# Kernel tuning notes

Measured on AMD Instinct MI355X. Metric: run time of the kernel, lower is better.

Reference implementation:

```python
import jax, jax.numpy as jnp
import numpy as np

D_MODEL = 512
D_STATE = 16
EPS = 1e-8
LN_EPS = 1e-5


def setup_inputs() -> dict:
    key = jax.random.key(0)
    ks = jax.random.split(key, 9)
    B, N = 4, 2048
    x = jax.random.normal(ks[0], (B, N, D_MODEL), dtype=jnp.float32)
    A_log = jax.random.normal(ks[1], (D_STATE,), dtype=jnp.float32) * 0.1 - 1.0
    # xavier_uniform with gain=0.5 for B and C linear weights
    lim_B = 0.5 * np.sqrt(6.0 / (D_MODEL + D_STATE))
    W_B = jax.random.uniform(ks[2], (D_STATE, D_MODEL), jnp.float32, -lim_B, lim_B)
    W_C = jax.random.uniform(ks[3], (D_MODEL, D_STATE), jnp.float32, -lim_B, lim_B)
    D = jax.random.normal(ks[4], (D_MODEL,), dtype=jnp.float32) * 0.01
    lim_g = np.sqrt(1.0 / D_MODEL)  # torch Linear default init
    W_gate = jax.random.uniform(ks[5], (D_MODEL, D_MODEL), jnp.float32, -lim_g, lim_g)
    b_gate = jax.random.uniform(ks[6], (D_MODEL,), jnp.float32, -lim_g, lim_g)
    ln_gamma = jnp.ones((D_MODEL,), jnp.float32)
    ln_beta = jnp.zeros((D_MODEL,), jnp.float32)
    return {"x": x, "A_log": A_log, "W_B": W_B, "W_C": W_C, "D": D,
            "W_gate": W_gate, "b_gate": b_gate, "ln_gamma": ln_gamma, "ln_beta": ln_beta}


def reference(x, A_log, W_B, W_C, D, W_gate, b_gate, ln_gamma, ln_beta):
    Bb, N, Dm = x.shape
    A = -jnp.clip(jnp.exp(A_log), EPS, 10.0)                      # (d_state,)
    dt = 1.0 / N
    A_bar = jnp.exp(dt * A)                                       # (d_state,)
    B_bar = jnp.where(jnp.abs(A) > EPS, (A_bar - 1.0) / (A + EPS),
                      jnp.full_like(A, dt))
    Bu = jnp.einsum('bnm,sm->bns', x, W_B) * B_bar                # (B,N,d_state)
    idx = jnp.arange(N)
    diff = jnp.clip(idx[None, :] - idx[:, None], 0, None)[..., None]  # (N,N,1)
    decay = A_bar[None, None, :] ** diff                          # (N,N,d_state)
    mask = (idx[None, :] >= idx[:, None])[..., None]
    decay = decay * mask.astype(decay.dtype)
    h = jnp.einsum('nms,bns->bms', decay, Bu)                     # (B,N,d_state)
    h = jnp.clip(h, -10.0, 10.0)
    y = jnp.einsum('bns,ms->bnm', h, W_C) + D * x                 # (B,N,d_model)
    gate = jax.nn.sigmoid(jnp.einsum('bnm,km->bnk', x, W_gate) + b_gate)
    y = gate * y + (1.0 - gate) * x
    # LayerNorm (dropout is identity in eval mode)
    mu = jnp.mean(y, axis=-1, keepdims=True)
    var = jnp.var(y, axis=-1, keepdims=True)
    return (y - mu) / jnp.sqrt(var + LN_EPS) * ln_gamma + ln_beta
```

## Files before the change

kernel.cpp:

```cpp
#include <hip/hip_runtime.h>
#include <math.h>
#include <stdint.h>

#define D_MODEL 512
#define D_STATE 16
#define NSEQ    2048
#define NBATCH  4
#define EPSF    1e-8f
#define LN_EPSF 1e-5f

typedef __attribute__((ext_vector_type(8))) short short8;
typedef __attribute__((ext_vector_type(4))) float floatx4;

__device__ __forceinline__ ushort f2bf(float f) {
    uint32_t u = __float_as_uint(f);
    return (ushort)((u + 0x7fffu + ((u >> 16) & 1u)) >> 16);
}

__global__ __launch_bounds__(256) void kA(const float* __restrict__ x,
                                          const float* __restrict__ A_log,
                                          const float* __restrict__ W_B,
                                          const float* __restrict__ Wg,
                                          ushort* __restrict__ wgb,
                                          float* __restrict__ Bu) {
    __shared__ float wb[D_STATE][D_MODEL + 4];
    const int tid = threadIdx.x;

    if (blockIdx.x < 128) {
        int i = blockIdx.x * 256 + tid;
        const float4* s = (const float4*)Wg + (size_t)i * 2;
        float4 a = s[0], b = s[1];
        float v[8] = {a.x, a.y, a.z, a.w, b.x, b.y, b.z, b.w};
        short8 o;
        #pragma unroll
        for (int j = 0; j < 8; ++j) o[j] = (short)f2bf(v[j]);
        *(short8*)(wgb + (size_t)i * 8) = o;
        return;
    }

    const float dt = 1.0f / (float)NSEQ;
    for (int i = tid; i < D_STATE * D_MODEL; i += 256) {
        int s = i / D_MODEL, m = i - s * D_MODEL;
        float A    = -fminf(fmaxf(expf(A_log[s]), EPSF), 10.0f);
        float Abar = expf(A * dt);
        float Bbar = (fabsf(A) > EPSF) ? (Abar - 1.0f) / (A + EPSF) : dt;
        wb[s][m] = W_B[i] * Bbar;
    }
    __syncthreads();

    const int lane = tid & 63, wave = tid >> 6;
    const int s    = lane & 15;
    const int rloc = (lane >> 4) + (wave << 2);
    const int row  = (blockIdx.x - 128) * 16 + rloc;
    const float* xr = x + (size_t)row * D_MODEL;

    float acc = 0.f;
    #pragma unroll 4
    for (int m = 0; m < D_MODEL; m += 4) {
        float4 xv = *(const float4*)(xr + m);
        float4 wv = *(const float4*)(&wb[s][m]);
        acc += xv.x * wv.x + xv.y * wv.y + xv.z * wv.z + xv.w * wv.w;
    }
    int b = row / NSEQ, n = row - b * NSEQ;
    Bu[((size_t)b * D_STATE + s) * NSEQ + n] = acc;
}

__global__ __launch_bounds__(256) void k2_scan(const float* __restrict__ Bu,
                                               const float* __restrict__ A_log,
                                               float* __restrict__ hT) {
    __shared__ float buf[NSEQ];
    __shared__ float wpair[8];
    const int bs = blockIdx.x;
    const int s  = bs & 15;
    const float dt = 1.0f / (float)NSEQ;
    float A    = -fminf(fmaxf(expf(A_log[s]), EPSF), 10.0f);
    float abar = expf(A * dt);

    const int tid = threadIdx.x;
    const float* src = Bu + (size_t)bs * NSEQ;
    for (int i = tid; i < NSEQ; i += 256) buf[i] = src[i];
    __syncthreads();

    const int n0 = tid * 8;
    float hh = 0.f;
    #pragma unroll
    for (int j = 0; j < 8; ++j) hh = abar * hh + buf[n0 + j];

    float a = abar * abar; a = a * a; a = a * a;
    float bseg = hh;

    const int lane = tid & 63, wave = tid >> 6;
    #pragma unroll
    for (int off = 1; off < 64; off <<= 1) {
        float ap = __shfl_up(a, off);
        float bp = __shfl_up(bseg, off);
        if (lane >= off) { bseg = a * bp + bseg; a = a * ap; }
    }
    if (lane == 63) { wpair[wave * 2] = a; wpair[wave * 2 + 1] = bseg; }
    __syncthreads();

    float pb = 0.f;
    for (int w = 0; w < wave; ++w) {
        float wa = wpair[w * 2], wbv = wpair[w * 2 + 1];
        pb = wa * pb + wbv;
    }
    float la = __shfl_up(a, 1), lb = __shfl_up(bseg, 1);
    if (lane == 0) { la = 1.f; lb = 0.f; }
    float hin = la * pb + lb;

    hh = hin;
    float outv[8];
    #pragma unroll
    for (int j = 0; j < 8; ++j) {
        hh = abar * hh + buf[n0 + j];
        outv[j] = fminf(fmaxf(hh, -10.f), 10.f);
    }
    __syncthreads();
    #pragma unroll
    for (int j = 0; j < 8; ++j) buf[n0 + j] = outv[j];
    __syncthreads();

    float* dst = hT + (size_t)bs * NSEQ;
    for (int i = tid; i < NSEQ; i += 256) dst[i] = buf[i];
}

#define CBM 16
#define BKC 32
__global__ __launch_bounds__(256) void kc_fused(
    const float*  __restrict__ x,
    const ushort* __restrict__ Wg,
    const float*  __restrict__ hT,
    const float*  __restrict__ W_C,
    const float*  __restrict__ Dvec,
    const float*  __restrict__ bg,
    const float*  __restrict__ gamma,
    const float*  __restrict__ beta,
    float* __restrict__ out) {
    __shared__ ushort Bsub[512 * BKC];
    __shared__ ushort Asub[CBM * BKC];
    __shared__ ushort wcs[512 * 16];
    __shared__ ushort hs[CBM * 16];
    __shared__ float  red[4][CBM][2];

    const int tid  = threadIdx.x;
    const int lane = tid & 63, wave = tid >> 6;
    const int r0   = blockIdx.x * CBM;
    const int fr   = lane & 15, kg = lane >> 4;
    const int colw = wave * 128;

    #pragma unroll
    for (int it = 0; it < 4; ++it) {
        int idx = it * 256 + tid;
        int row = idx >> 1, g = idx & 1;
        const float4* src = (const float4*)(W_C + (size_t)row * D_STATE + g * 8);
        float4 v0 = src[0], v1 = src[1];
        float v[8] = {v0.x,v0.y,v0.z,v0.w,v1.x,v1.y,v1.z,v1.w};
        short8 o;
        #pragma unroll
        for (int e = 0; e < 8; ++e) o[e] = (short)f2bf(v[e]);
        *(short8*)(wcs + row * 16 + (g ^ (row & 1)) * 8) = o;
    }
    {
        int s = tid & 15, nloc = tid >> 4;
        int b = r0 >> 11, n0 = r0 & (NSEQ - 1);
        float hv = hT[((size_t)b * D_STATE + s) * NSEQ + n0 + nloc];
        int g = s >> 3;
        hs[nloc * 16 + (g ^ (nloc & 1)) * 8 + (s & 7)] = f2bf(hv);
    }

    floatx4 acc[8] = {};
    const int arow = tid >> 4;
    const int akp  = (tid & 15) * 2;

    for (int kc = 0; kc < D_MODEL; kc += BKC) {
        const float* axp = x + (size_t)(r0 + arow) * D_MODEL + kc + akp;
        float2 av = *(const float2*)axp;

        __syncthreads();

        {
            int g = akp >> 3;
            int addr = arow * BKC + ((g ^ (arow & 3)) * 8) + (akp & 7);
            ushort2 o; o.x = f2bf(av.x); o.y = f2bf(av.y);
            *(ushort2*)(Asub + addr) = o;
        }
        #pragma unroll
        for (int is = 0; is < 8; ++is) {
            int row = is * 64 + (tid >> 2);
            int g   = (tid & 3) ^ (row & 3);
            const ushort* gsrc = Wg + (size_t)row * D_MODEL + kc + g * 8;
            __builtin_amdgcn_global_load_lds(
                (const __attribute__((address_space(1))) void*)gsrc,
                (__attribute__((address_space(3))) void*)((char*)Bsub + is * 4096 + tid * 16),
                16, 0, 0);
        }
        __syncthreads();

        short8 af = *(const short8*)(Asub + fr * BKC + ((kg ^ (fr & 3)) * 8));
        #pragma unroll
        for (int j = 0; j < 8; ++j) {
            int rb = colw + j * 16 + fr;
            short8 bv = *(const short8*)(Bsub + (size_t)rb * BKC + ((kg ^ (rb & 3)) * 8));
            acc[j] = __builtin_amdgcn_mfma_f32_16x16x32_bf16(af, bv, acc[j], 0, 0, 0);
        }
    }

    const short8 z8 = short8{0,0,0,0,0,0,0,0};
    short8 ah = (kg < 2) ? *(const short8*)(hs + fr * 16 + ((kg ^ (fr & 1)) * 8)) : z8;
    floatx4 yc[8] = {};
    #pragma unroll
    for (int j = 0; j < 8; ++j) {
        int rb = colw + j * 16 + fr;
        short8 bw = (kg < 2) ? *(const short8*)(wcs + rb * 16 + ((kg ^ (rb & 1)) * 8)) : z8;
        yc[j] = __builtin_amdgcn_mfma_f32_16x16x32_bf16(ah, bw, yc[j], 0, 0, 0);
    }

    float vsum[4] = {}, vsq[4] = {};
    #pragma unroll
    for (int j = 0; j < 8; ++j) {
        int col = colw + j * 16 + fr;
        float dv = Dvec[col], bgv = bg[col];
        #pragma unroll
        for (int q = 0; q < 4; ++q) {
            int rl = kg * 4 + q;
            float xv = x[(size_t)(r0 + rl) * D_MODEL + col];
            float lg = acc[j][q] + bgv;
            float gt = 1.f / (1.f + expf(-lg));
            float yv = yc[j][q] + dv * xv;
            float v  = gt * yv + (1.f - gt) * xv;
            acc[j][q] = v;
            vsum[q] += v;
            vsq[q]  += v * v;
        }
    }
    #pragma unroll
    for (int off = 1; off < 16; off <<= 1) {
        #pragma unroll
        for (int q = 0; q < 4; ++q) {
            vsum[q] += __shfl_xor(vsum[q], off);
            vsq[q]  += __shfl_xor(vsq[q], off);
        }
    }
    if (fr == 0) {
        #pragma unroll
        for (int q = 0; q < 4; ++q) {
            red[wave][kg * 4 + q][0] = vsum[q];
            red[wave][kg * 4 + q][1] = vsq[q];
        }
    }
    __syncthreads();
    float mu[4], rs[4];
    #pragma unroll
    for (int q = 0; q < 4; ++q) {
        int rl = kg * 4 + q;
        float s = 0.f, ss = 0.f;
        #pragma unroll
        for (int w = 0; w < 4; ++w) { s += red[w][rl][0]; ss += red[w][rl][1]; }
        float m   = s * (1.f / (float)D_MODEL);
        float var = ss * (1.f / (float)D_MODEL) - m * m;
        mu[q] = m;
        rs[q] = rsqrtf(var + LN_EPSF);
    }
    #pragma unroll
    for (int j = 0; j < 8; ++j) {
        int col = colw + j * 16 + fr;
        float ga = gamma[col], be = beta[col];
        #pragma unroll
        for (int q = 0; q < 4; ++q)
            out[(size_t)(r0 + kg * 4 + q) * D_MODEL + col] =
                (acc[j][q] - mu[q]) * rs[q] * ga + be;
    }
}

extern "C" void kernel_launch(void* const* d_in, const int* in_sizes, int n_in,
                              void* d_out, int out_size, void* d_ws, size_t ws_size,
                              hipStream_t stream) {
    const float* x     = (const float*)d_in[0];
    const float* A_log = (const float*)d_in[1];
    const float* W_B   = (const float*)d_in[2];
    const float* W_C   = (const float*)d_in[3];
    const float* Dv    = (const float*)d_in[4];
    const float* Wg    = (const float*)d_in[5];
    const float* bg    = (const float*)d_in[6];
    const float* gamma = (const float*)d_in[7];
    const float* beta  = (const float*)d_in[8];
    float* out = (float*)d_out;

    const int rows = NBATCH * NSEQ;

    ushort* wgb = (ushort*)d_ws;
    float*  Bu  = (float*)(wgb + (size_t)D_MODEL * D_MODEL);
    float*  hT  = Bu + (size_t)NBATCH * D_STATE * NSEQ;

    hipLaunchKernelGGL(kA,      dim3(128 + rows / 16),  dim3(256), 0, stream,
                       x, A_log, W_B, Wg, wgb, Bu);
    hipLaunchKernelGGL(k2_scan, dim3(NBATCH * D_STATE), dim3(256), 0, stream, Bu, A_log, hT);
    hipLaunchKernelGGL(kc_fused, dim3(rows / CBM),      dim3(256), 0, stream,
                       x, wgb, hT, W_C, Dv, bg, gamma, beta, out);
}
```

Measured before the change: 51.97 us.

## Fuse scan into projection kernel via chunked local scans and carry propagation

Removes the separate scan kernel. Each projection block now computes a local 16-row scan of Bu using wave shuffles and writes per-row local states plus a chunk-end state. The fused output kernel rebuilds the incoming carry by serially combining up to 127 earlier chunk states, then adds the decayed carry to the local state before clamping. The bf16 conversion of W_gate is spread across all projection blocks. This saves a kernel launch and the Bu/hT round trip, but adds a serial prefix loop of up to 127 steps per block in the fused kernel.

Result: faster. 47.01 us (median of 2 runs) (-9.6%).

```diff
diff --git a/kernel.cpp b/kernel.cpp
--- a/kernel.cpp
+++ b/kernel.cpp
@@ -8,6 +8,7 @@
 #define NBATCH  4
 #define EPSF    1e-8f
 #define LN_EPSF 1e-5f
+#define DT      (1.0f / 2048.0f)
 
 typedef __attribute__((ext_vector_type(8))) short short8;
 typedef __attribute__((ext_vector_type(4))) float floatx4;
@@ -17,41 +18,45 @@
     return (ushort)((u + 0x7fffu + ((u >> 16) & 1u)) >> 16);
 }
 
-__global__ __launch_bounds__(256) void kA(const float* __restrict__ x,
+__global__ __launch_bounds__(256) void kP(const float* __restrict__ x,
                                           const float* __restrict__ A_log,
                                           const float* __restrict__ W_B,
                                           const float* __restrict__ Wg,
                                           ushort* __restrict__ wgb,
-                                          float* __restrict__ Bu) {
+                                          float* __restrict__ hL,
+                                          float* __restrict__ states) {
     __shared__ float wb[D_STATE][D_MODEL + 4];
-    const int tid = threadIdx.x;
-
-    if (blockIdx.x < 128) {
-        int i = blockIdx.x * 256 + tid;
-        const float4* s = (const float4*)Wg + (size_t)i * 2;
-        float4 a = s[0], b = s[1];
+    __shared__ float bbars[16], abars[16];
+    __shared__ float w4[4][16];
+    const int tid = threadIdx.x, lane = tid & 63, wave = tid >> 6;
+
+    if (tid < 64) {
+        int i = blockIdx.x * 64 + tid;
+        const float4* sp = (const float4*)Wg + (size_t)i * 2;
+        float4 a = sp[0], b = sp[1];
         float v[8] = {a.x, a.y, a.z, a.w, b.x, b.y, b.z, b.w};
         short8 o;
         #pragma unroll
         for (int j = 0; j < 8; ++j) o[j] = (short)f2bf(v[j]);
         *(short8*)(wgb + (size_t)i * 8) = o;
-        return;
-    }
-
-    const float dt = 1.0f / (float)NSEQ;
+    }
+    if (tid < 16) {
+        float A    = -fminf(fmaxf(expf(A_log[tid]), EPSF), 10.0f);
+        float Abar = expf(A * DT);
+        abars[tid] = Abar;
+        bbars[tid] = (fabsf(A) > EPSF) ? (Abar - 1.0f) / (A + EPSF) : DT;
+    }
+    __syncthreads();
     for (int i = tid; i < D_STATE * D_MODEL; i += 256) {
-        int s = i / D_MODEL, m = i - s * D_MODEL;
-        float A    = -fminf(fmaxf(expf(A_log[s]), EPSF), 10.0f);
-        float Abar = expf(A * dt);
-        float Bbar = (fabsf(A) > EPSF) ? (Abar - 1.0f) / (A + EPSF) : dt;
-        wb[s][m] = W_B[i] * Bbar;
-    }
-    __syncthreads();
-
-    const int lane = tid & 63, wave = tid >> 6;
+        int s = i >> 9, m = i & 511;
+        wb[s][m] = W_B[i] * bbars[s];
+    }
+    __syncthreads();
+
     const int s    = lane & 15;
-    const int rloc = (lane >> 4) + (wave << 2);
-    const int row  = (blockIdx.x - 128) * 16 + rloc;
+    const int q    = lane >> 4;
+    const int rloc = q + (wave << 2);
+    const int row  = blockIdx.x * 16 + rloc;
     const float* xr = x + (size_t)row * D_MODEL;
 
     float acc = 0.f;
@@ -61,67 +66,26 @@
         float4 wv = *(const float4*)(&wb[s][m]);
         acc += xv.x * wv.x + xv.y * wv.y + xv.z * wv.z + xv.w * wv.w;
     }
-    int b = row / NSEQ, n = row - b * NSEQ;
-    Bu[((size_t)b * D_STATE + s) * NSEQ + n] = acc;
-}
-
-__global__ __launch_bounds__(256) void k2_scan(const float* __restrict__ Bu,
-                                               const float* __restrict__ A_log,
-                                               float* __restrict__ hT) {
-    __shared__ float buf[NSEQ];
-    __shared__ float wpair[8];
-    const int bs = blockIdx.x;
-    const int s  = bs & 15;
-    const float dt = 1.0f / (float)NSEQ;
-    float A    = -fminf(fmaxf(expf(A_log[s]), EPSF), 10.0f);
-    float abar = expf(A * dt);
-
-    const int tid = threadIdx.x;
-    const float* src = Bu + (size_t)bs * NSEQ;
-    for (int i = tid; i < NSEQ; i += 256) buf[i] = src[i];
-    __syncthreads();
-
-    const int n0 = tid * 8;
-    float hh = 0.f;
-    #pragma unroll
-    for (int j = 0; j < 8; ++j) hh = abar * hh + buf[n0 + j];
-
-    float a = abar * abar; a = a * a; a = a * a;
-    float bseg = hh;
-
-    const int lane = tid & 63, wave = tid >> 6;
-    #pragma unroll
-    for (int off = 1; off < 64; off <<= 1) {
-        float ap = __shfl_up(a, off);
-        float bp = __shfl_up(bseg, off);
-        if (lane >= off) { bseg = a * bp + bseg; a = a * ap; }
-    }
-    if (lane == 63) { wpair[wave * 2] = a; wpair[wave * 2 + 1] = bseg; }
-    __syncthreads();
-
+
+    float abar = abars[s];
+    float a = abar, b = acc;
+    {
+        float ap = __shfl_up(a, 16), bp = __shfl_up(b, 16);
+        if (lane >= 16) { b = a * bp + b; a = a * ap; }
+    }
+    {
+        float ap = __shfl_up(a, 32), bp = __shfl_up(b, 32);
+        if (lane >= 32) { b = a * bp + b; a = a * ap; }
+    }
+    if (q == 3) w4[wave][s] = b;
+    __syncthreads();
+    float a4 = abar * abar; a4 = a4 * a4;
     float pb = 0.f;
-    for (int w = 0; w < wave; ++w) {
-        float wa = wpair[w * 2], wbv = wpair[w * 2 + 1];
-        pb = wa * pb + wbv;
-    }
-    float la = __shfl_up(a, 1), lb = __shfl_up(bseg, 1);
-    if (lane == 0) { la = 1.f; lb = 0.f; }
-    float hin = la * pb + lb;
-
-    hh = hin;
-    float outv[8];
-    #pragma unroll
-    for (int j = 0; j < 8; ++j) {
-        hh = abar * hh + buf[n0 + j];
-        outv[j] = fminf(fmaxf(hh, -10.f), 10.f);
-    }
-    __syncthreads();
-    #pragma unroll
-    for (int j = 0; j < 8; ++j) buf[n0 + j] = outv[j];
-    __syncthreads();
-
-    float* dst = hT + (size_t)bs * NSEQ;
-    for (int i = tid; i < NSEQ; i += 256) dst[i] = buf[i];
+    for (int w = 0; w < wave; ++w) pb = a4 * pb + w4[w][s];
+    float hloc = a * pb + b;
+
+    hL[(size_t)row * D_STATE + s] = hloc;
+    if (rloc == 15) states[(size_t)blockIdx.x * D_STATE + s] = hloc;
 }
 
 #define CBM 16
@@ -129,7 +93,9 @@
 __global__ __launch_bounds__(256) void kc_fused(
     const float*  __restrict__ x,
     const ushort* __restrict__ Wg,
-    const float*  __restrict__ hT,
+    const float*  __restrict__ hL,
+    const float*  __restrict__ states,
+    const float*  __restrict__ A_log,
     const float*  __restrict__ W_C,
     const float*  __restrict__ Dvec,
     const float*  __restrict__ bg,
@@ -137,8 +103,8 @@
     const float*  __restrict__ beta,
     float* __restrict__ out) {
     __shared__ ushort Bsub[512 * BKC];
+    __shared__ ushort wcs[512 * 16];
     __shared__ ushort Asub[CBM * BKC];
-    __shared__ ushort wcs[512 * 16];
     __shared__ ushort hs[CBM * 16];
     __shared__ float  red[4][CBM][2];
 
@@ -147,6 +113,11 @@
     const int r0   = blockIdx.x * CBM;
     const int fr   = lane & 15, kg = lane >> 4;
     const int colw = wave * 128;
+
+    float* stg = (float*)Bsub;
+    const int c0 = blockIdx.x & 127;
+    for (int i = tid; i < c0 * 16; i += 256)
+        stg[i] = states[(size_t)(blockIdx.x - c0) * 16 + i];
 
     #pragma unroll
     for (int it = 0; it < 4; ++it) {
@@ -160,12 +131,18 @@
         for (int e = 0; e < 8; ++e) o[e] = (short)f2bf(v[e]);
         *(short8*)(wcs + row * 16 + (g ^ (row & 1)) * 8) = o;
     }
+    __syncthreads();
+
     {
         int s = tid & 15, nloc = tid >> 4;
-        int b = r0 >> 11, n0 = r0 & (NSEQ - 1);
-        float hv = hT[((size_t)b * D_STATE + s) * NSEQ + n0 + nloc];
-        int g = s >> 3;
-        hs[nloc * 16 + (g ^ (nloc & 1)) * 8 + (s & 7)] = f2bf(hv);
+        float A   = -fminf(fmaxf(expf(A_log[s]), EPSF), 10.0f);
+        float a16 = expf(A * DT * 16.0f);
+        float p = 0.f;
+        for (int cc = 0; cc < c0; ++cc) p = a16 * p + stg[cc * 16 + s];
+        float hv = expf(A * DT * (float)(nloc + 1)) * p
+                 + hL[(size_t)(r0 + nloc) * D_STATE + s];
+        hv = fminf(fmaxf(hv, -10.f), 10.f);
+        hs[nloc * 16 + (((s >> 3) ^ (nloc & 1)) * 8) + (s & 7)] = f2bf(hv);
     }
 
     floatx4 acc[8] = {};
@@ -288,13 +265,12 @@
 
     const int rows = NBATCH * NSEQ;
 
-    ushort* wgb = (ushort*)d_ws;
-    float*  Bu  = (float*)(wgb + (size_t)D_MODEL * D_MODEL);
-    float*  hT  = Bu + (size_t)NBATCH * D_STATE * NSEQ;
-
-    hipLaunchKernelGGL(kA,      dim3(128 + rows / 16),  dim3(256), 0, stream,
-                       x, A_log, W_B, Wg, wgb, Bu);
-    hipLaunchKernelGGL(k2_scan, dim3(NBATCH * D_STATE), dim3(256), 0, stream, Bu, A_log, hT);
-    hipLaunchKernelGGL(kc_fused, dim3(rows / CBM),      dim3(256), 0, stream,
-                       x, wgb, hT, W_C, Dv, bg, gamma, beta, out);
-}
+    ushort* wgb    = (ushort*)d_ws;
+    float*  hL     = (float*)(wgb + (size_t)D_MODEL * D_MODEL);
+    float*  states = hL + (size_t)rows * D_STATE;
+
+    hipLaunchKernelGGL(kP, dim3(rows / 16), dim3(256), 0, stream,
+                       x, A_log, W_B, Wg, wgb, hL, states);
+    hipLaunchKernelGGL(kc_fused, dim3(rows / CBM), dim3(256), 0, stream,
+                       x, wgb, hL, states, A_log, W_C, Dv, bg, gamma, beta, out);
+}
```
